# Kernel tuning notes

Hardware: AMD Instinct MI355X
Metric: run time of the kernel (lower is better)

The kernel has to match this reference:

```python
import jax, jax.numpy as jnp
from jax import lax
import numpy as np

D_MODEL = 1024
D_STATE = 16
D_CONV = 4
EXPAND = 2
D_INNER = EXPAND * D_MODEL  # 2048
DT_RANK = D_MODEL // 16     # 64
BATCH = 2
SEQLEN = 1024


def setup_inputs() -> dict:
    key = jax.random.key(0)
    ks = iter(jax.random.split(key, 32))

    def nrm(shape, s=0.02):
        return jax.random.normal(next(ks), shape, jnp.float32) * s

    def mamba_params():
        return dict(
            Win=nrm((2 * D_INNER, D_MODEL)), bin=jnp.zeros((2 * D_INNER,), jnp.float32),
            convw=nrm((D_INNER, D_CONV), 0.1), convb=jnp.zeros((D_INNER,), jnp.float32),
            Wx=nrm((DT_RANK + 2 * D_STATE, D_INNER)),
            Wdt=nrm((D_INNER, DT_RANK), 0.1), bdt=nrm((D_INNER,), 0.1),
            Alog=jnp.log(jnp.broadcast_to(jnp.arange(1, D_STATE + 1, dtype=jnp.float32), (D_INNER, D_STATE))),
            Dsk=jnp.ones((D_INNER,), jnp.float32),
            Wout=nrm((D_MODEL, D_INNER)), bout=jnp.zeros((D_MODEL,), jnp.float32),
        )

    inp = {"x": jax.random.normal(next(ks), (BATCH, SEQLEN, D_MODEL), jnp.float32)}
    for pref, p in (("f_", mamba_params()), ("b_", mamba_params())):
        for k, v in p.items():
            inp[pref + k] = v
    inp["proj_W"] = nrm((D_MODEL, 2 * D_MODEL))
    inp["proj_b"] = jnp.zeros((D_MODEL,), jnp.float32)
    return inp


def selective_scan(u, delta, A, Bm, Cm, Dsk):
    # u, delta: (B,L,Di); Bm, Cm: (B,L,N); A: (Di,N); Dsk: (Di,)
    def step(h, inp):
        u_t, d_t, b_t, c_t = inp  # (B,Di),(B,Di),(B,N),(B,N)
        dA = jnp.exp(d_t[..., None] * A)                      # (B,Di,N)
        h = h * dA + (d_t * u_t)[..., None] * b_t[:, None, :]  # (B,Di,N)
        y = jnp.einsum('bdn,bn->bd', h, c_t)
        return h, y

    h0 = jnp.zeros((u.shape[0], A.shape[0], A.shape[1]), u.dtype)
    xs = (u.transpose(1, 0, 2), delta.transpose(1, 0, 2),
          Bm.transpose(1, 0, 2), Cm.transpose(1, 0, 2))
    _, ys = lax.scan(step, h0, xs)
    return ys.transpose(1, 0, 2) + u * Dsk  # (B,L,Di)


def mamba_fwd(x, Win, bin_, convw, convb, Wx, Wdt, bdt, Alog, Dsk, Wout, bout):
    xz = x @ Win.T + bin_                      # (B,L,2*Di)
    xin, z = jnp.split(xz, 2, axis=-1)
    # causal depthwise conv over time: (B,Di,L)
    xc = lax.conv_general_dilated(
        xin.transpose(0, 2, 1), convw[:, None, :], (1,), [(D_CONV - 1, 0)],
        dimension_numbers=('NCH', 'OIH', 'NCH'), feature_group_count=D_INNER)
    u = jax.nn.silu(xc.transpose(0, 2, 1) + convb)  # (B,L,Di)
    xdbl = u @ Wx.T                                 # (B,L,dt_rank+2N)
    dt, Bm, Cm = jnp.split(xdbl, [DT_RANK, DT_RANK + D_STATE], axis=-1)
    delta = jax.nn.softplus(dt @ Wdt.T + bdt)       # (B,L,Di)
    A = -jnp.exp(Alog)
    y = selective_scan(u, delta, A, Bm, Cm, Dsk)
    y = y * jax.nn.silu(z)
    return y @ Wout.T + bout


def reference(x,
              f_Win, f_bin, f_convw, f_convb, f_Wx, f_Wdt, f_bdt, f_Alog, f_Dsk, f_Wout, f_bout,
              b_Win, b_bin, b_convw, b_convb, b_Wx, b_Wdt, b_bdt, b_Alog, b_Dsk, b_Wout, b_bout,
              proj_W, proj_b):
    out_f = mamba_fwd(x, f_Win, f_bin, f_convw, f_convb, f_Wx, f_Wdt, f_bdt, f_Alog, f_Dsk, f_Wout, f_bout)
    xr = jnp.flip(x, axis=1)
    out_b = mamba_fwd(xr, b_Win, b_bin, b_convw, b_convb, b_Wx, b_Wdt, b_bdt, b_Alog, b_Dsk, b_Wout, b_bout)
    out_b = jnp.flip(out_b, axis=1)
    out = jnp.concatenate([out_f, out_b], axis=-1)  # (B,L,2*d_model)
    return out @ proj_W.T + proj_b
```

## Files before the change

### kernel.cpp

```cpp
#include <hip/hip_runtime.h>
#include <math.h>

#define D_MODEL 1024
#define D_STATE 16
#define D_CONV  4
#define D_INNER 2048
#define DT_RANK 64
#define BATCH   2
#define SEQLEN  1024
#define MROWS   2048
#define XDBL_LD 128
#define NCHUNK  32
#define CLEN    (SEQLEN / NCHUNK)
#define NCHG    8192

typedef __attribute__((ext_vector_type(8))) short bf16x8;
typedef __attribute__((ext_vector_type(4))) float f32x4;

#define BARR() asm volatile("s_barrier" ::: "memory")
#define VMW(n) asm volatile("s_waitcnt vmcnt(" #n ")" ::: "memory")

static __device__ __forceinline__ float sigmoidf_(float x) {
    return 1.f / (1.f + __expf(-x));
}
static __device__ __forceinline__ unsigned short bf16rn(float f) {
    unsigned u = __float_as_uint(f);
    return (unsigned short)((u + 0x7FFFu + ((u >> 16) & 1u)) >> 16);
}
static __device__ __forceinline__ void hl_split(float f, unsigned short& h, unsigned short& l) {
    h = bf16rn(f);
    l = bf16rn(f - __uint_as_float((unsigned)h << 16));
}
static __device__ __forceinline__ float us2f(unsigned short u) {
    return __uint_as_float((unsigned)u << 16);
}

static __device__ __forceinline__
void split_block(const float* __restrict__ in, int R, int C, int ldin,
                 unsigned short* __restrict__ out, int Rout, bool flip,
                 int blk, int tid)
{
    int q = blk * 256 + tid;
    int qpr = C >> 2;
    int row = q / qpr;
    int c4 = (q - row * qpr) << 2;
    if (row >= Rout) return;
    unsigned short h[4] = {0, 0, 0, 0}, l[4] = {0, 0, 0, 0};
    if (row < R) {
        int sr = row;
        if (flip) { int b = row >> 10, t = row & 1023; sr = (b << 10) + (1023 - t); }
        float4 v = *(const float4*)(in + (size_t)sr * ldin + c4);
        float f[4] = {v.x, v.y, v.z, v.w};
        #pragma unroll
        for (int i = 0; i < 4; ++i) hl_split(f[i], h[i], l[i]);
    }
    size_t ob = (size_t)row * (2 * C);
    *(ushort4*)(out + ob + c4)     = make_ushort4(h[0], h[1], h[2], h[3]);
    *(ushort4*)(out + ob + C + c4) = make_ushort4(l[0], l[1], l[2], l[3]);
}

__global__ __launch_bounds__(256)
void prep1_kernel(const float* __restrict__ x,
                  const float* __restrict__ Win0, const float* __restrict__ Win1,
                  const float* __restrict__ Wx0,  const float* __restrict__ Wx1,
                  const float* __restrict__ Wdt0, const float* __restrict__ Wdt1,
                  unsigned short* xc0,
                  unsigned short* Winb0, unsigned short* Winb1,
                  unsigned short* Wxb0, unsigned short* Wxb1,
                  unsigned short* Wdtb0, unsigned short* Wdtb1)
{
    int b = blockIdx.x, tid = threadIdx.x;
    if      (b < 2048)  split_block(x,    MROWS, D_MODEL, D_MODEL, xc0,  MROWS, false, b,        tid);
    else if (b < 6144)  split_block(Win0, 4096,  D_MODEL, D_MODEL, Winb0, 4096, false, b - 2048, tid);
    else if (b < 10240) split_block(Win1, 4096,  D_MODEL, D_MODEL, Winb1, 4096, false, b - 6144, tid);
    else if (b < 10496) split_block(Wx0,  96,    D_INNER, D_INNER, Wxb0,  128,  false, b - 10240, tid);
    else if (b < 10752) split_block(Wx1,  96,    D_INNER, D_INNER, Wxb1,  128,  false, b - 10496, tid);
    else if (b < 10880) split_block(Wdt0, D_INNER, DT_RANK, DT_RANK, Wdtb0, D_INNER, false, b - 10752, tid);
    else                split_block(Wdt1, D_INNER, DT_RANK, DT_RANK, Wdtb1, D_INNER, false, b - 10880, tid);
}

#define SWZ(row) (((row) >> 1) & 3)
#define RDA(p, kk, row) (*(const bf16x8*)&AS[p][kk][row][(fs ^ SWZ(row)) << 3])
#define RDB(p, kk, row) (*(const bf16x8*)&BS[p][kk][row][(fs ^ SWZ(row)) << 3])

#define KTILE(MODE, kt) do { \
    const int p_ = (kt) & 1; \
    bf16x8 bF[4]; \
    {  \
        bf16x8 aF[4]; \
        _Pragma("unroll") for (int f = 0; f < 4; ++f) { int rw = wm + f * 16 + fr; aF[f] = RDA(p_, 0, rw); } \
        _Pragma("unroll") for (int g = 0; g < 4; ++g) { int rw = wn + g * 16 + fr; bF[g] = RDB(p_, 0, rw); } \
        if (MODE < 2) stageA((kt) + 1, 1); \
        BARR(); __builtin_amdgcn_s_setprio(1); \
        _Pragma("unroll") for (int f = 0; f < 4; ++f) \
        _Pragma("unroll") for (int g = 0; g < 4; ++g) \
            acc[f][g] = __builtin_amdgcn_mfma_f32_16x16x32_bf16(aF[f], bF[g], acc[f][g], 0, 0, 0); \
        __builtin_amdgcn_s_setprio(0); \
    } \
    {  \
        bf16x8 aF[4]; \
        _Pragma("unroll") for (int f = 0; f < 4; ++f) { int rw = wm + 64 + f * 16 + fr; aF[f] = RDA(p_, 0, rw); } \
        if (MODE == 0) stageB((kt) + 2, 0); \
        BARR(); __builtin_amdgcn_s_setprio(1); \
        _Pragma("unroll") for (int f = 0; f < 4; ++f) \
        _Pragma("unroll") for (int g = 0; g < 4; ++g) \
            acc[4 + f][g] = __builtin_amdgcn_mfma_f32_16x16x32_bf16(aF[f], bF[g], acc[4 + f][g], 0, 0, 0); \
        __builtin_amdgcn_s_setprio(0); \
    } \
    {  \
        bf16x8 aF[4]; \
        _Pragma("unroll") for (int f = 0; f < 4; ++f) { int rw = wm + f * 16 + fr; aF[f] = RDA(p_, 1, rw); } \
        _Pragma("unroll") for (int g = 0; g < 4; ++g) { int rw = wn + g * 16 + fr; bF[g] = RDB(p_, 1, rw); } \
        if (MODE == 0) stageA((kt) + 2, 0); \
        BARR(); __builtin_amdgcn_s_setprio(1); \
        _Pragma("unroll") for (int f = 0; f < 4; ++f) \
        _Pragma("unroll") for (int g = 0; g < 4; ++g) \
            acc[f][g] = __builtin_amdgcn_mfma_f32_16x16x32_bf16(aF[f], bF[g], acc[f][g], 0, 0, 0); \
        __builtin_amdgcn_s_setprio(0); \
    } \
    {  \
        if (MODE == 0) { VMW(4); } else if (MODE == 1) { VMW(0); } \
        bf16x8 aF[4]; \
        _Pragma("unroll") for (int f = 0; f < 4; ++f) { int rw = wm + 64 + f * 16 + fr; aF[f] = RDA(p_, 1, rw); } \
        if (MODE == 0) stageB((kt) + 2, 1); \
        BARR(); __builtin_amdgcn_s_setprio(1); \
        _Pragma("unroll") for (int f = 0; f < 4; ++f) \
        _Pragma("unroll") for (int g = 0; g < 4; ++g) \
            acc[4 + f][g] = __builtin_amdgcn_mfma_f32_16x16x32_bf16(aF[f], bF[g], acc[4 + f][g], 0, 0, 0); \
        __builtin_amdgcn_s_setprio(0); \
    } \
} while (0)

template<int ACT, bool PART, int KTS, bool DUALN>
__global__ __launch_bounds__(512, 1)
void gemm256(const unsigned short* __restrict__ A0,
             const unsigned short* __restrict__ A1,
             const unsigned short* __restrict__ W0,
             const unsigned short* __restrict__ W1,
             const float* __restrict__ bias0,
             const float* __restrict__ bias1,
             float* __restrict__ C0, float* __restrict__ C1,
             float* __restrict__ part,
             int ldc, int N, int K, int nks)
{
    __shared__ unsigned short AS[2][2][256][32];
    __shared__ unsigned short BS[2][2][256][32];

    const int tid = threadIdx.x;
    const int lane = tid & 63;
    const int wid = tid >> 6;

    const int z = blockIdx.z;
    const int zdir = z / nks;
    const int ks = z - zdir * nks;

    const int nbx = gridDim.x;
    const int nwg = nbx * gridDim.y;
    int bid = blockIdx.y * nbx + blockIdx.x;
    int q8 = nwg >> 3;
    int swz = (bid & 7) * q8 + (bid >> 3);
    const int bm = (swz / nbx) * 256;
    const int bn = (swz % nbx) * 256;

    int dn, bnn;
    if (DUALN) { dn = (bn >= (N >> 1)) ? 1 : 0; bnn = bn - dn * (N >> 1); }
    else       { dn = zdir; bnn = bn; }
    const unsigned short* A = (DUALN || dn == 0) ? A0 : A1;
    const unsigned short* W = dn ? W1 : W0;

    const int ldg = 2 * K;
    constexpr int NT = 3 * KTS;
    const int Kc = KTS * 64;
    const int kbase = ks * Kc;

    const int wm = (wid >> 2) * 128;
    const int wn = (wid & 3) * 64;
    const int fr = lane & 15;
    const int fs = lane >> 4;

    f32x4 acc[8][4];
    #pragma unroll
    for (int i = 0; i < 8; ++i)
        #pragma unroll
        for (int j = 0; j < 4; ++j) {
            f32x4 zv = {0.f, 0.f, 0.f, 0.f};
            acc[i][j] = zv;
        }

    auto koffA = [&](int t) { unsigned tu = (unsigned)t; unsigned sg = tu / KTS;
                              unsigned w = tu - sg * KTS;
                              return (int)((sg == 1 ? (unsigned)K : 0u) + kbase + w * 64); };
    auto koffB = [&](int t) { unsigned tu = (unsigned)t; unsigned sg = tu / KTS;
                              unsigned w = tu - sg * KTS;
                              return (int)((sg == 2 ? (unsigned)K : 0u) + kbase + w * 64); };

    auto stageA = [&](int t, int kk) {
        int ko = koffA(t) + kk * 32;
        unsigned short* dst = &AS[t & 1][kk][0][0];
        #pragma unroll
        for (int i = 0; i < 2; ++i) {
            int s = i * 512 + tid;
            int row = s >> 2, sl = s & 3, lsl = sl ^ SWZ(row);
            const unsigned short* src = A + (size_t)(bm + row) * ldg + ko + lsl * 8;
            __builtin_amdgcn_global_load_lds(
                (const __attribute__((address_space(1))) void*)src,
                (__attribute__((address_space(3))) void*)(dst + s * 8), 16, 0, 0);
        }
    };
    auto stageB = [&](int t, int kk) {
        int ko = koffB(t) + kk * 32;
        unsigned short* dst = &BS[t & 1][kk][0][0];
        #pragma unroll
        for (int i = 0; i < 2; ++i) {
            int s = i * 512 + tid;
            int row = s >> 2, sl = s & 3, lsl = sl ^ SWZ(row);
            const unsigned short* src = W + (size_t)(bnn + row) * ldg + ko + lsl * 8;
            __builtin_amdgcn_global_load_lds(
                (const __attribute__((address_space(1))) void*)src,
                (__attribute__((address_space(3))) void*)(dst + s * 8), 16, 0, 0);
        }
    };

    stageB(0, 0); stageA(0, 0); stageB(0, 1); stageA(0, 1);
    stageB(1, 0); stageA(1, 0); stageB(1, 1);
    VMW(6);
    BARR();

    #pragma unroll 1
    for (int kt = 0; kt < NT - 2; ++kt) KTILE(0, kt);
    KTILE(1, NT - 2);
    KTILE(2, NT - 1);

    if (PART) {
        float* P = part + (size_t)z * ((size_t)MROWS * N);
        #pragma unroll
        for (int i = 0; i < 8; ++i)
            #pragma unroll
            for (int j = 0; j < 4; ++j) {
                int coln = bnn + wn + j * 16 + fr;
                #pragma unroll
                for (int r = 0; r < 4; ++r) {
                    int rowm = bm + wm + i * 16 + fs * 4 + r;
                    P[(size_t)rowm * N + coln] = acc[i][j][r];
                }
            }
    } else {
        const float* bias = dn ? bias1 : bias0;
        float* C = dn ? C1 : C0;
        #pragma unroll
        for (int i = 0; i < 8; ++i)
            #pragma unroll
            for (int j = 0; j < 4; ++j) {
                int coln = bnn + wn + j * 16 + fr;
                float bv = bias ? bias[coln] : 0.f;
                #pragma unroll
                for (int r = 0; r < 4; ++r) {
                    int rowm = bm + wm + i * 16 + fs * 4 + r;
                    float v = acc[i][j][r] + bv;
                    if (ACT == 1) v = (v > 20.f) ? v : log1pf(__expf(v));
                    int crow = rowm;
                    if (DUALN && dn) { int bb = rowm >> 10, t = rowm & 1023; crow = (bb << 10) + 1023 - t; }
                    C[(size_t)crow * ldc + coln] = v;
                }
            }
    }
}

template<int ACT, bool PART>
__global__ __launch_bounds__(256)
void gemm_mfma(const unsigned short* __restrict__ A0,
               const unsigned short* __restrict__ A1,
               const unsigned short* __restrict__ W0,
               const unsigned short* __restrict__ W1,
               const float* __restrict__ bias0,
               const float* __restrict__ bias1,
               float* __restrict__ C0, float* __restrict__ C1,
               float* __restrict__ part,
               int ldc, int N, int K, int nks)
{
    __shared__ __align__(16) unsigned short As[128 * 32];
    __shared__ __align__(16) unsigned short Bs[128 * 32];

    const int tid = threadIdx.x;
    const int lane = tid & 63;
    const int wid = tid >> 6;

    const int z = blockIdx.z;
    const int dir = z / nks;
    const int ks = z - dir * nks;
    const unsigned short* A = dir ? A1 : A0;
    const unsigned short* W = dir ? W1 : W0;

    const int nbx = gridDim.x;
    const int nwg = nbx * gridDim.y;
    int bid = blockIdx.y * nbx + blockIdx.x;
    int q8 = nwg >> 3;
    int swz = (nwg >= 8) ? (bid & 7) * q8 + (bid >> 3) : bid;
    const int bm = (swz / nbx) * 128;
    const int bn = (swz % nbx) * 128;

    const int ldg = 2 * K;
    const int Kc = K / nks;
    const int kbase = ks * Kc;

    f32x4 acc[4][4];
    #pragma unroll
    for (int i = 0; i < 4; ++i)
        #pragma unroll
        for (int j = 0; j < 4; ++j) {
            f32x4 zv = {0.f, 0.f, 0.f, 0.f};
            acc[i][j] = zv;
        }

    const int r0 = tid >> 2;
    const int k0s = (tid & 3) ^ ((r0 >> 1) & 3);
    const int r1 = (256 + tid) >> 2;
    const int k1s = (tid & 3) ^ ((r1 >> 1) & 3);

    unsigned short* As_w0 = &As[(wid << 6) * 8];
    unsigned short* As_w1 = &As[(256 + (wid << 6)) * 8];
    unsigned short* Bs_w0 = &Bs[(wid << 6) * 8];
    unsigned short* Bs_w1 = &Bs[(256 + (wid << 6)) * 8];

    const int wm = (wid >> 1) * 64;
    const int wn = (wid & 1) * 64;
    const int fr = lane & 15;
    const int fs = lane >> 4;

    const int KS = Kc >> 5;
    #pragma unroll 1
    for (int seg = 0; seg < 3; ++seg) {
        const int aoff = ((seg == 1) ? K : 0) + kbase;
        const int boff = ((seg == 2) ? K : 0) + kbase;
        #pragma unroll 1
        for (int kt = 0; kt < KS; ++kt) {
            const int kk = kt << 5;
            const unsigned short* ga0 = A + (size_t)(bm + r0) * ldg + aoff + kk + k0s * 8;
            const unsigned short* ga1 = A + (size_t)(bm + r1) * ldg + aoff + kk + k1s * 8;
            const unsigned short* gw0 = W + (size_t)(bn + r0) * ldg + boff + kk + k0s * 8;
            const unsigned short* gw1 = W + (size_t)(bn + r1) * ldg + boff + kk + k1s * 8;
            __builtin_amdgcn_global_load_lds(
                (const __attribute__((address_space(1))) void*)ga0,
                (__attribute__((address_space(3))) void*)As_w0, 16, 0, 0);
            __builtin_amdgcn_global_load_lds(
                (const __attribute__((address_space(1))) void*)ga1,
                (__attribute__((address_space(3))) void*)As_w1, 16, 0, 0);
            __builtin_amdgcn_global_load_lds(
                (const __attribute__((address_space(1))) void*)gw0,
                (__attribute__((address_space(3))) void*)Bs_w0, 16, 0, 0);
            __builtin_amdgcn_global_load_lds(
                (const __attribute__((address_space(1))) void*)gw1,
                (__attribute__((address_space(3))) void*)Bs_w1, 16, 0, 0);
            __syncthreads();

            bf16x8 aF[4], bF[4];
            #pragma unroll
            for (int f = 0; f < 4; ++f) {
                int ra = wm + f * 16 + fr;
                int sa = fs ^ ((ra >> 1) & 3);
                aF[f] = *(const bf16x8*)&As[ra * 32 + sa * 8];
                int rb = wn + f * 16 + fr;
                int sb = fs ^ ((rb >> 1) & 3);
                bF[f] = *(const bf16x8*)&Bs[rb * 32 + sb * 8];
            }
            #pragma unroll
            for (int i = 0; i < 4; ++i)
                #pragma unroll
                for (int j = 0; j < 4; ++j)
                    acc[i][j] = __builtin_amdgcn_mfma_f32_16x16x32_bf16(
                        aF[i], bF[j], acc[i][j], 0, 0, 0);
            __syncthreads();
        }
    }

    if (PART) {
        float* P = part + (size_t)z * ((size_t)MROWS * N);
        #pragma unroll
        for (int i = 0; i < 4; ++i)
            #pragma unroll
            for (int j = 0; j < 4; ++j) {
                int coln = bn + wn + j * 16 + fr;
                #pragma unroll
                for (int r = 0; r < 4; ++r) {
                    int rowm = bm + wm + i * 16 + fs * 4 + r;
                    P[(size_t)rowm * N + coln] = acc[i][j][r];
                }
            }
    } else {
        const float* bias = dir ? bias1 : bias0;
        float* C = dir ? C1 : C0;
        #pragma unroll
        for (int i = 0; i < 4; ++i)
            #pragma unroll
            for (int j = 0; j < 4; ++j) {
                int coln = bn + wn + j * 16 + fr;
                float bv = bias ? bias[coln] : 0.f;
                #pragma unroll
                for (int r = 0; r < 4; ++r) {
                    int rowm = bm + wm + i * 16 + fs * 4 + r;
                    float v = acc[i][j][r] + bv;
                    if (ACT == 1) v = (v > 20.f) ? v : log1pf(__expf(v));
                    C[(size_t)rowm * ldc + coln] = v;
                }
            }
    }
}

__global__ __launch_bounds__(256)
void reduce_xdbl_k(const float* __restrict__ part,
                   float* __restrict__ xdbl0, float* __restrict__ xdbl1,
                   unsigned short* __restrict__ dtb0, unsigned short* __restrict__ dtb1)
{
    const int dz = blockIdx.z;
    const float* P = part + (size_t)dz * 16 * MROWS * XDBL_LD;
    float* xdbl = dz ? xdbl1 : xdbl0;
    unsigned short* dtb = dz ? dtb1 : dtb0;
    int i = blockIdx.x * 256 + threadIdx.x;
    int row = i >> 5;
    int c4 = (i & 31) << 2;
    float4 s = make_float4(0.f, 0.f, 0.f, 0.f);
    #pragma unroll
    for (int k = 0; k < 16; ++k) {
        float4 v = *(const float4*)(P + (size_t)k * MROWS * XDBL_LD + (size_t)row * XDBL_LD + c4);
        s.x += v.x; s.y += v.y; s.z += v.z; s.w += v.w;
    }
    *(float4*)(xdbl + (size_t)row * XDBL_LD + c4) = s;
    if (c4 < DT_RANK) {
        float f[4] = {s.x, s.y, s.z, s.w};
        unsigned short h[4], l[4];
        #pragma unroll
        for (int j = 0; j < 4; ++j) hl_split(f[j], h[j], l[j]);
        *(ushort4*)(dtb + (size_t)row * (2 * DT_RANK) + c4) = make_ushort4(h[0], h[1], h[2], h[3]);
        *(ushort4*)(dtb + (size_t)row * (2 * DT_RANK) + DT_RANK + c4) = make_ushort4(l[0], l[1], l[2], l[3]);
    }
}

__global__ __launch_bounds__(256)
void mid_kernel(const float* __restrict__ part2,
                const float* __restrict__ bout0, const float* __restrict__ bout1,
                unsigned short* __restrict__ tmpb,
                const float* __restrict__ projW, unsigned short* __restrict__ pWb)
{
    const int dz = blockIdx.z;
    const int tid = threadIdx.x;
    if (dz == 2) {
        split_block(projW, D_MODEL, 2 * D_MODEL, 2 * D_MODEL, pWb, D_MODEL, false, blockIdx.x, tid);
        return;
    }
    const float* P = part2 + (size_t)dz * 4 * MROWS * D_MODEL;
    const float* bias = dz ? bout1 : bout0;
    const int colofs = dz ? D_MODEL : 0;
    int i = blockIdx.x * 256 + tid;
    int row = i >> 8;
    int c4 = (i & 255) << 2;
    float4 s = make_float4(bias[c4], bias[c4 + 1], bias[c4 + 2], bias[c4 + 3]);
    #pragma unroll
    for (int k = 0; k < 4; ++k) {
        float4 v = *(const float4*)(P + (size_t)k * MROWS * D_MODEL + (size_t)row * D_MODEL + c4);
        s.x += v.x; s.y += v.y; s.z += v.z; s.w += v.w;
    }
    int orow = row;
    if (dz) { int bb = row >> 10, t = row & 1023; orow = (bb << 10) + 1023 - t; }
    float f[4] = {s.x, s.y, s.z, s.w};
    unsigned short h[4], l[4];
    #pragma unroll
    for (int j = 0; j < 4; ++j) hl_split(f[j], h[j], l[j]);
    *(ushort4*)(tmpb + (size_t)orow * 4096 + colofs + c4) = make_ushort4(h[0], h[1], h[2], h[3]);
    *(ushort4*)(tmpb + (size_t)orow * 4096 + 2048 + colofs + c4) = make_ushort4(l[0], l[1], l[2], l[3]);
}

__global__ __launch_bounds__(256)
void reduce_out_k(const float* __restrict__ part, const float* __restrict__ bias,
                  float* __restrict__ out)
{
    int i = blockIdx.x * 256 + threadIdx.x;
    int row = i >> 8;
    int c4 = (i & 255) << 2;
    float4 s = make_float4(bias[c4], bias[c4 + 1], bias[c4 + 2], bias[c4 + 3]);
    #pragma unroll
    for (int k = 0; k < 8; ++k) {
        float4 v = *(const float4*)(part + (size_t)k * MROWS * D_MODEL + (size_t)row * D_MODEL + c4);
        s.x += v.x; s.y += v.y; s.z += v.z; s.w += v.w;
    }
    *(float4*)(out + (size_t)row * D_MODEL + c4) = s;
}

__global__ __launch_bounds__(256)
void conv_prep_kernel(const float* __restrict__ xz0, const float* __restrict__ xz1,
                      const float* __restrict__ cw0, const float* __restrict__ cw1,
                      const float* __restrict__ cb0, const float* __restrict__ cb1,
                      unsigned short* __restrict__ ub0, unsigned short* __restrict__ ub1,
                      const float* __restrict__ Wout0, const float* __restrict__ Wout1,
                      unsigned short* __restrict__ Woutb0, unsigned short* __restrict__ Woutb1)
{
    const int dz = blockIdx.z;
    const int tid = threadIdx.x;
    if (dz == 2) {
        int b = blockIdx.x;
        if (b < 2048) split_block(Wout0, D_MODEL, D_INNER, D_INNER, Woutb0, D_MODEL, false, b, tid);
        else if (b < 4096) split_block(Wout1, D_MODEL, D_INNER, D_INNER, Woutb1, D_MODEL, false, b - 2048, tid);
        return;
    }
    const float* xz = dz ? xz1 : xz0;
    const float* convw = dz ? cw1 : cw0;
    const float* convb = dz ? cb1 : cb0;
    unsigned short* ub = dz ? ub1 : ub0;
    int idx = blockIdx.x * 256 + tid;
    int d = idx % D_INNER;
    int r = idx / D_INNER;
    int t = r % SEQLEN;
    float acc = convb[d];
    #pragma unroll
    for (int k = 0; k < D_CONV; ++k) {
        int back = D_CONV - 1 - k;
        if (t - back >= 0)
            acc += xz[(size_t)(r - back) * (2 * D_INNER) + d] * convw[d * D_CONV + k];
    }
    float v = acc * sigmoidf_(acc);
    unsigned short h, l;
    hl_split(v, h, l);
    ub[(size_t)r * (2 * D_INNER) + d] = h;
    ub[(size_t)r * (2 * D_INNER) + D_INNER + d] = l;
}

__global__ __launch_bounds__(256)
void scan_phase1(const float* __restrict__ delta0, const float* __restrict__ delta1,
                 const unsigned short* __restrict__ ub0, const unsigned short* __restrict__ ub1,
                 const float* __restrict__ xdbl0, const float* __restrict__ xdbl1,
                 const float* __restrict__ Alog0, const float* __restrict__ Alog1,
                 float* __restrict__ aprod, float* __restrict__ hfin)
{
    const int gid = blockIdx.x * 256 + threadIdx.x;
    const int chg = gid & (NCHG - 1);
    const int chunk = gid >> 13;
    const int dir = chg >> 12;
    const int bd = chg & 4095;
    const int b = bd >> 11, d = bd & 2047;
    const float* delta = dir ? delta1 : delta0;
    const unsigned short* ub = dir ? ub1 : ub0;
    const float* xdbl = dir ? xdbl1 : xdbl0;
    const float* Alog = dir ? Alog1 : Alog0;

    float Av[16], h[16], ap[16];
    #pragma unroll
    for (int n = 0; n < 16; ++n) {
        Av[n] = -__expf(Alog[d * D_STATE + n]);
        h[n] = 0.f; ap[n] = 1.f;
    }
    const int t0 = chunk * CLEN;
    for (int t = t0; t < t0 + CLEN; ++t) {
        const size_t r = (size_t)b * SEQLEN + t;
        float dlt = delta[r * D_INNER + d];
        float uu = us2f(ub[r * 4096 + d]) + us2f(ub[r * 4096 + 2048 + d]);
        float du = dlt * uu;
        float4 bq[4];
        #pragma unroll
        for (int q = 0; q < 4; ++q)
            bq[q] = *(const float4*)(xdbl + r * XDBL_LD + DT_RANK + q * 4);
        #pragma unroll
        for (int n = 0; n < 16; ++n) {
            float Bv = ((const float*)&bq[n >> 2])[n & 3];
            float dA = __expf(dlt * Av[n]);
            h[n] = h[n] * dA + du * Bv;
            ap[n] *= dA;
        }
    }
    float* pa = aprod + (size_t)chunk * (NCHG * 16) + (size_t)chg * 16;
    float* pf = hfin  + (size_t)chunk * (NCHG * 16) + (size_t)chg * 16;
    #pragma unroll
    for (int q = 0; q < 4; ++q) {
        *(float4*)(pa + q * 4) = make_float4(ap[q*4], ap[q*4+1], ap[q*4+2], ap[q*4+3]);
        *(float4*)(pf + q * 4) = make_float4(h[q*4], h[q*4+1], h[q*4+2], h[q*4+3]);
    }
}

__global__ __launch_bounds__(256)
void scan_phase2(float* __restrict__ aprod ,
                 const float* __restrict__ hfin)
{
    const int gid = blockIdx.x * 256 + threadIdx.x;
    float h = 0.f;
    for (int c = 0; c < NCHUNK; ++c) {
        const size_t idx = (size_t)c * (NCHG * 16) + gid;
        float a = aprod[idx];
        float f = hfin[idx];
        aprod[idx] = h;
        h = a * h + f;
    }
}

__global__ __launch_bounds__(256)
void scan_phase3(const float* __restrict__ delta0, const float* __restrict__ delta1,
                 unsigned short* __restrict__ ub0, unsigned short* __restrict__ ub1,
                 const float* __restrict__ xdbl0, const float* __restrict__ xdbl1,
                 const float* __restrict__ Alog0, const float* __restrict__ Alog1,
                 const float* __restrict__ Dsk0, const float* __restrict__ Dsk1,
                 const float* __restrict__ xz0, const float* __restrict__ xz1,
                 const float* __restrict__ hin)
{
    const int gid = blockIdx.x * 256 + threadIdx.x;
    const int chg = gid & (NCHG - 1);
    const int chunk = gid >> 13;
    const int dir = chg >> 12;
    const int bd = chg & 4095;
    const int b = bd >> 11, d = bd & 2047;
    const float* delta = dir ? delta1 : delta0;
    unsigned short* ub = dir ? ub1 : ub0;
    const float* xdbl = dir ? xdbl1 : xdbl0;
    const float* Alog = dir ? Alog1 : Alog0;
    const float* Dsk = dir ? Dsk1 : Dsk0;
    const float* xz = dir ? xz1 : xz0;

    float Av[16], h[16];
    const float* ph = hin + (size_t)chunk * (NCHG * 16) + (size_t)chg * 16;
    #pragma unroll
    for (int n = 0; n < 16; ++n) {
        Av[n] = -__expf(Alog[d * D_STATE + n]);
        h[n] = ph[n];
    }
    const float Dv = Dsk[d];
    const int t0 = chunk * CLEN;
    for (int t = t0; t < t0 + CLEN; ++t) {
        const size_t r = (size_t)b * SEQLEN + t;
        float dlt = delta[r * D_INNER + d];
        float uu = us2f(ub[r * 4096 + d]) + us2f(ub[r * 4096 + 2048 + d]);
        float du = dlt * uu;
        float4 bq[4], cq[4];
        #pragma unroll
        for (int q = 0; q < 4; ++q) {
            bq[q] = *(const float4*)(xdbl + r * XDBL_LD + DT_RANK + q * 4);
            cq[q] = *(const float4*)(xdbl + r * XDBL_LD + DT_RANK + D_STATE + q * 4);
        }
        float p0 = 0.f, p1 = 0.f, p2 = 0.f, p3 = 0.f;
        #pragma unroll
        for (int n = 0; n < 16; ++n) {
            float Bv = ((const float*)&bq[n >> 2])[n & 3];
            float Cv = ((const float*)&cq[n >> 2])[n & 3];
            float dA = __expf(dlt * Av[n]);
            h[n] = h[n] * dA + du * Bv;
            if ((n & 3) == 0) p0 += h[n] * Cv;
            else if ((n & 3) == 1) p1 += h[n] * Cv;
            else if ((n & 3) == 2) p2 += h[n] * Cv;
            else p3 += h[n] * Cv;
        }
        float y = ((p0 + p1) + (p2 + p3)) + uu * Dv;
        float zv = xz[r * (2 * D_INNER) + D_INNER + d];
        float v = y * (zv * sigmoidf_(zv));
        unsigned short hh, ll;
        hl_split(v, hh, ll);
        ub[r * 4096 + d] = hh;
        ub[r * 4096 + 2048 + d] = ll;
    }
}

extern "C" void kernel_launch(void* const* d_in, const int* in_sizes, int n_in,
                              void* d_out, int out_size, void* d_ws, size_t ws_size,
                              hipStream_t stream)
{
    const float* x = (const float*)d_in[0];
    const float* proj_W = (const float*)d_in[23];
    const float* proj_b = (const float*)d_in[24];
    float* out = (float*)d_out;

    const float *Win[2], *bin_[2], *convw[2], *convb[2], *Wx[2], *Wdt[2], *bdt[2],
                *Alog[2], *Dsk[2], *Wout[2], *bout[2];
    for (int dir = 0; dir < 2; ++dir) {
        const int base = 1 + dir * 11;
        Win[dir]   = (const float*)d_in[base + 0];
        bin_[dir]  = (const float*)d_in[base + 1];
        convw[dir] = (const float*)d_in[base + 2];
        convb[dir] = (const float*)d_in[base + 3];
        Wx[dir]    = (const float*)d_in[base + 4];
        Wdt[dir]   = (const float*)d_in[base + 5];
        bdt[dir]   = (const float*)d_in[base + 6];
        Alog[dir]  = (const float*)d_in[base + 7];
        Dsk[dir]   = (const float*)d_in[base + 8];
        Wout[dir]  = (const float*)d_in[base + 9];
        bout[dir]  = (const float*)d_in[base + 10];
    }

    char* ws = (char*)d_ws;
    const size_t MB = 1ull << 20;
    float* xz[2]            = {(float*)(ws + 0 * MB),   (float*)(ws + 32 * MB)};
    unsigned short* ub[2]   = {(unsigned short*)(ws + 64 * MB),
                               (unsigned short*)(ws + 80 * MB)};
    unsigned short* Winb[2] = {(unsigned short*)(ws + 96 * MB),
                               (unsigned short*)(ws + 112 * MB)};
    unsigned short* xc0     = (unsigned short*)(ws + 128 * MB);
    float* part             = (float*)(ws + 112 * MB);
    float* part2            = (float*)(ws + 0 * MB);
    float* delta[2]         = {(float*)(ws + 112 * MB), (float*)(ws + 128 * MB)};
    unsigned short* Woutb[2]= {(unsigned short*)(ws + 96 * MB),
                               (unsigned short*)(ws + 104 * MB)};
    unsigned short* yzb[2]  = {ub[0], ub[1]};
    unsigned short* tmpb    = ub[0];
    unsigned short* pWb     = ub[1];
    unsigned short* Wxb[2]  = {(unsigned short*)(ws + 144 * MB), (unsigned short*)(ws + 145 * MB)};
    unsigned short* Wdtb[2] = {(unsigned short*)(ws + 146 * MB), (unsigned short*)(ws + 146 * MB + 512 * 1024)};
    unsigned short* dtb[2]  = {(unsigned short*)(ws + 147 * MB), (unsigned short*)(ws + 147 * MB + 512 * 1024)};
    float* xdbl[2]          = {(float*)(ws + 148 * MB), (float*)(ws + 149 * MB)};
    float* aprod            = (float*)(ws + 150 * MB);
    float* hfin             = (float*)(ws + 167 * MB);

    dim3 blk(256);

    prep1_kernel<<<11008, blk, 0, stream>>>(
        x, Win[0], Win[1], Wx[0], Wx[1], Wdt[0], Wdt[1],
        xc0, Winb[0], Winb[1], Wxb[0], Wxb[1], Wdtb[0], Wdtb[1]);

    gemm256<0, false, 16, true><<<dim3(32, 8, 1), dim3(512), 0, stream>>>(
        xc0, nullptr, Winb[0], Winb[1], bin_[0], bin_[1], xz[0], xz[1],
        nullptr, 4096, 8192, D_MODEL, 1);

    conv_prep_kernel<<<dim3((MROWS * D_INNER) / 256, 1, 3), blk, 0, stream>>>(
        xz[0], xz[1], convw[0], convw[1], convb[0], convb[1], ub[0], ub[1],
        Wout[0], Wout[1], Woutb[0], Woutb[1]);

    gemm_mfma<0, true><<<dim3(1, 16, 32), blk, 0, stream>>>(
        ub[0], ub[1], Wxb[0], Wxb[1], nullptr, nullptr, nullptr, nullptr,
        part, XDBL_LD, XDBL_LD, D_INNER, 16);

    reduce_xdbl_k<<<dim3(256, 1, 2), blk, 0, stream>>>(
        part, xdbl[0], xdbl[1], dtb[0], dtb[1]);

    gemm_mfma<1, false><<<dim3(16, 16, 2), blk, 0, stream>>>(
        dtb[0], dtb[1], Wdtb[0], Wdtb[1], bdt[0], bdt[1], delta[0], delta[1],
        nullptr, D_INNER, D_INNER, DT_RANK, 1);

    scan_phase1<<<NCHUNK * NCHG / 256, blk, 0, stream>>>(
        delta[0], delta[1], ub[0], ub[1], xdbl[0], xdbl[1], Alog[0], Alog[1],
        aprod, hfin);
    scan_phase2<<<NCHG * 16 / 256, blk, 0, stream>>>(aprod, hfin);
    scan_phase3<<<NCHUNK * NCHG / 256, blk, 0, stream>>>(
        delta[0], delta[1], ub[0], ub[1], xdbl[0], xdbl[1], Alog[0], Alog[1],
        Dsk[0], Dsk[1], xz[0], xz[1], aprod);

    gemm256<0, true, 8, false><<<dim3(4, 8, 8), dim3(512), 0, stream>>>(
        yzb[0], yzb[1], Woutb[0], Woutb[1], nullptr, nullptr, nullptr, nullptr,
        part2, D_MODEL, D_MODEL, D_INNER, 4);

    mid_kernel<<<dim3(2048, 1, 3), blk, 0, stream>>>(
        part2, bout[0], bout[1], tmpb, proj_W, pWb);

    gemm256<0, true, 4, false><<<dim3(4, 8, 8), dim3(512), 0, stream>>>(
        tmpb, nullptr, pWb, nullptr, nullptr, nullptr, nullptr, nullptr,
        part2, D_MODEL, D_MODEL, 2 * D_MODEL, 8);

    reduce_out_k<<<2048, blk, 0, stream>>>(part2, proj_b, out);
}
```

Measured before the change: 471.4 us.

## Software-pipeline LDS fragment reads against MFMA in the 256-tile GEMM

Restructures the GEMM k-tile loop so the A/B fragment reads from LDS for the next sub-step are issued right after each barrier. The current MFMA block runs while those reads are in flight, using double-buffered register fragments (aFA/aFB/bFA/bFB), partial lgkmcnt waits and sched_barriers to stop the compiler from reordering. The first fragments are preloaded before the loop, and the last sub-step of each tile prefetches the next tile's first fragments. A separate GEMM kernel also changes its LDS write base pointers from a per-wave base to a per-thread row/slot address. Holding more live fragment registers raises VGPR pressure, and the hand-placed waits must match the real number of outstanding LDS ops or results will be wrong.

```diff
diff --git a/kernel.cpp b/kernel.cpp
--- a/kernel.cpp
+++ b/kernel.cpp
@@ -19,6 +19,8 @@
 
 #define BARR() asm volatile("s_barrier" ::: "memory")
 #define VMW(n) asm volatile("s_waitcnt vmcnt(" #n ")" ::: "memory")
+#define LGKM(n) asm volatile("s_waitcnt lgkmcnt(" #n ")" ::: "memory")
+#define SCHB() __builtin_amdgcn_sched_barrier(0)
 
 static __device__ __forceinline__ float sigmoidf_(float x) {
     return 1.f / (1.f + __expf(-x));
@@ -83,50 +85,54 @@
 #define RDA(p, kk, row) (*(const bf16x8*)&AS[p][kk][row][(fs ^ SWZ(row)) << 3])
 #define RDB(p, kk, row) (*(const bf16x8*)&BS[p][kk][row][(fs ^ SWZ(row)) << 3])
 
+#define MFMA16(ACCBASE, AF, BF) \
+    _Pragma("unroll") for (int f = 0; f < 4; ++f) \
+    _Pragma("unroll") for (int g = 0; g < 4; ++g) \
+        acc[(ACCBASE) + f][g] = __builtin_amdgcn_mfma_f32_16x16x32_bf16(AF[f], BF[g], acc[(ACCBASE) + f][g], 0, 0, 0);
+
 #define KTILE(MODE, kt) do { \
     const int p_ = (kt) & 1; \
-    bf16x8 bF[4]; \
+    const int pn_ = ((kt) + 1) & 1; \
     {  \
-        bf16x8 aF[4]; \
-        _Pragma("unroll") for (int f = 0; f < 4; ++f) { int rw = wm + f * 16 + fr; aF[f] = RDA(p_, 0, rw); } \
-        _Pragma("unroll") for (int g = 0; g < 4; ++g) { int rw = wn + g * 16 + fr; bF[g] = RDB(p_, 0, rw); } \
         if (MODE < 2) stageA((kt) + 1, 1); \
-        BARR(); __builtin_amdgcn_s_setprio(1); \
-        _Pragma("unroll") for (int f = 0; f < 4; ++f) \
-        _Pragma("unroll") for (int g = 0; g < 4; ++g) \
-            acc[f][g] = __builtin_amdgcn_mfma_f32_16x16x32_bf16(aF[f], bF[g], acc[f][g], 0, 0, 0); \
+        BARR(); \
+        _Pragma("unroll") for (int f = 0; f < 4; ++f) { int rw = wm + 64 + f * 16 + fr; aFB[f] = RDA(p_, 0, rw); } \
+        LGKM(4); SCHB(); \
+        __builtin_amdgcn_s_setprio(1); \
+        MFMA16(0, aFA, bFA) \
         __builtin_amdgcn_s_setprio(0); \
     } \
     {  \
-        bf16x8 aF[4]; \
-        _Pragma("unroll") for (int f = 0; f < 4; ++f) { int rw = wm + 64 + f * 16 + fr; aF[f] = RDA(p_, 0, rw); } \
         if (MODE == 0) stageB((kt) + 2, 0); \
-        BARR(); __builtin_amdgcn_s_setprio(1); \
-        _Pragma("unroll") for (int f = 0; f < 4; ++f) \
-        _Pragma("unroll") for (int g = 0; g < 4; ++g) \
-            acc[4 + f][g] = __builtin_amdgcn_mfma_f32_16x16x32_bf16(aF[f], bF[g], acc[4 + f][g], 0, 0, 0); \
+        BARR(); \
+        _Pragma("unroll") for (int f = 0; f < 4; ++f) { int rw = wm + f * 16 + fr; aFA[f] = RDA(p_, 1, rw); } \
+        _Pragma("unroll") for (int g = 0; g < 4; ++g) { int rw = wn + g * 16 + fr; bFB[g] = RDB(p_, 1, rw); } \
+        LGKM(8); SCHB(); \
+        __builtin_amdgcn_s_setprio(1); \
+        MFMA16(4, aFB, bFA) \
         __builtin_amdgcn_s_setprio(0); \
     } \
     {  \
-        bf16x8 aF[4]; \
-        _Pragma("unroll") for (int f = 0; f < 4; ++f) { int rw = wm + f * 16 + fr; aF[f] = RDA(p_, 1, rw); } \
-        _Pragma("unroll") for (int g = 0; g < 4; ++g) { int rw = wn + g * 16 + fr; bF[g] = RDB(p_, 1, rw); } \
         if (MODE == 0) stageA((kt) + 2, 0); \
-        BARR(); __builtin_amdgcn_s_setprio(1); \
-        _Pragma("unroll") for (int f = 0; f < 4; ++f) \
-        _Pragma("unroll") for (int g = 0; g < 4; ++g) \
-            acc[f][g] = __builtin_amdgcn_mfma_f32_16x16x32_bf16(aF[f], bF[g], acc[f][g], 0, 0, 0); \
+        BARR(); \
+        _Pragma("unroll") for (int f = 0; f < 4; ++f) { int rw = wm + 64 + f * 16 + fr; aFB[f] = RDA(p_, 1, rw); } \
+        LGKM(4); SCHB(); \
+        __builtin_amdgcn_s_setprio(1); \
+        MFMA16(0, aFA, bFB) \
         __builtin_amdgcn_s_setprio(0); \
     } \
     {  \
         if (MODE == 0) { VMW(4); } else if (MODE == 1) { VMW(0); } \
-        bf16x8 aF[4]; \
-        _Pragma("unroll") for (int f = 0; f < 4; ++f) { int rw = wm + 64 + f * 16 + fr; aF[f] = RDA(p_, 1, rw); } \
         if (MODE == 0) stageB((kt) + 2, 1); \
-        BARR(); __builtin_amdgcn_s_setprio(1); \
-        _Pragma("unroll") for (int f = 0; f < 4; ++f) \
-        _Pragma("unroll") for (int g = 0; g < 4; ++g) \
-            acc[4 + f][g] = __builtin_amdgcn_mfma_f32_16x16x32_bf16(aF[f], bF[g], acc[4 + f][g], 0, 0, 0); \
+        BARR(); \
+        if (MODE < 2) { \
+            _Pragma("unroll") for (int f = 0; f < 4; ++f) { int rw = wm + f * 16 + fr; aFA[f] = RDA(pn_, 0, rw); } \
+            _Pragma("unroll") for (int g = 0; g < 4; ++g) { int rw = wn + g * 16 + fr; bFA[g] = RDB(pn_, 0, rw); } \
+            LGKM(8); \
+        } else { LGKM(0); } \
+        SCHB(); \
+        __builtin_amdgcn_s_setprio(1); \
+        MFMA16(4, aFB, bFB) \
         __builtin_amdgcn_s_setprio(0); \
     } \
 } while (0)
@@ -225,6 +231,12 @@
     stageB(1, 0); stageA(1, 0); stageB(1, 1);
     VMW(6);
     BARR();
+
+    bf16x8 aFA[4], aFB[4], bFA[4], bFB[4];
+    #pragma unroll
+    for (int f = 0; f < 4; ++f) { int rw = wm + f * 16 + fr; aFA[f] = RDA(0, 0, rw); }
+    #pragma unroll
+    for (int g = 0; g < 4; ++g) { int rw = wn + g * 16 + fr; bFA[g] = RDB(0, 0, rw); }
 
     #pragma unroll 1
     for (int kt = 0; kt < NT - 2; ++kt) KTILE(0, kt);
@@ -317,10 +329,10 @@
     const int r1 = (256 + tid) >> 2;
     const int k1s = (tid & 3) ^ ((r1 >> 1) & 3);
 
-    unsigned short* As_w0 = &As[(wid << 6) * 8];
-    unsigned short* As_w1 = &As[(256 + (wid << 6)) * 8];
-    unsigned short* Bs_w0 = &Bs[(wid << 6) * 8];
-    unsigned short* Bs_w1 = &Bs[(256 + (wid << 6)) * 8];
+    unsigned short* As_w0 = &As[(tid >> 2) * 32 + ((tid & 3) << 3)];
+    unsigned short* As_w1 = As_w0 + 64 * 32;
+    unsigned short* Bs_w0 = &Bs[(tid >> 2) * 32 + ((tid & 3) << 3)];
+    unsigned short* Bs_w1 = Bs_w0 + 64 * 32;
 
     const int wm = (wid >> 1) * 64;
     const int wn = (wid & 1) * 64;
```

New measurement: 459.0 us. 2.6% less time.
